# Kernel optimization log

Hardware: AMD Instinct MI355X
Metric: run time of the kernel (lower is better)

The kernel has to match this reference:

```python
import jax, jax.numpy as jnp
import numpy as np

DIM = 512
HEADS = 8
HD = DIM // HEADS          # head_dim = 64
GROUPS = 32                # GroupNorm groups
EPS = 1e-5
SCALE = HD ** -0.25        # double-scale: applied to both q and k
B, H, W, L, CTX = 8, 32, 32, 77, 768


def setup_inputs() -> dict:
    key = jax.random.key(0)
    ks = jax.random.split(key, 6)
    return {
        "x": jax.random.normal(ks[0], (B, DIM, H, W), jnp.float32),
        "context": jax.random.normal(ks[1], (B, L, CTX), jnp.float32),
        "gn_gamma": jnp.ones((DIM,), jnp.float32),
        "gn_beta": jnp.zeros((DIM,), jnp.float32),
        "qkv_w": jax.random.normal(ks[2], (3 * DIM, DIM), jnp.float32) * 0.02,
        "qkv_b": jnp.zeros((3 * DIM,), jnp.float32),
        "ckv_w": jax.random.normal(ks[3], (2 * DIM, CTX), jnp.float32) * 0.02,
        "ckv_b": jnp.zeros((2 * DIM,), jnp.float32),
        "proj_w": jax.random.normal(ks[4], (DIM, DIM), jnp.float32) * 0.02,
        "proj_b": jnp.zeros((DIM,), jnp.float32),
    }


def _group_norm(x, gamma, beta):
    b, c, h, w = x.shape
    xr = x.reshape(b, GROUPS, c // GROUPS, h, w)
    mu = xr.mean(axis=(2, 3, 4), keepdims=True)
    var = xr.var(axis=(2, 3, 4), keepdims=True)
    xr = (xr - mu) * jax.lax.rsqrt(var + EPS)
    return xr.reshape(b, c, h, w) * gamma[None, :, None, None] + beta[None, :, None, None]


def reference(x, context, gn_gamma, gn_beta, qkv_w, qkv_b, ckv_w, ckv_b, proj_w, proj_b):
    b, c, h, w = x.shape
    n, d = HEADS, HD
    identity = x

    xn = _group_norm(x, gn_gamma, gn_beta)
    # 1x1 conv == channel GEMM. qkv: [b, 3*dim, h*w] -> [b, 3, n, d, hw]
    qkv = jnp.einsum('bchw,oc->bohw', xn, qkv_w) + qkv_b[None, :, None, None]
    qkv = qkv.reshape(b, 3, n, d, h * w)
    q, k, v = qkv[:, 0], qkv[:, 1], qkv[:, 2]   # each [b, n, d, hw]

    # context kv: Linear(context_dim, 2*dim) -> [b, L, 2, n, d] -> [b, n, d, L]
    ckv = jnp.einsum('blc,oc->blo', context, ckv_w) + ckv_b
    ckv = ckv.reshape(b, -1, 2, n, d)
    ck = jnp.transpose(ckv[:, :, 0], (0, 2, 3, 1))  # [b, n, d, L]
    cv = jnp.transpose(ckv[:, :, 1], (0, 2, 3, 1))
    k = jnp.concatenate([ck, k], axis=-1)           # [b, n, d, L+hw]
    v = jnp.concatenate([cv, v], axis=-1)

    # attn = (q^T * s) @ (k * s); softmax over keys
    attn = jnp.einsum('bndq,bndk->bnqk', q * SCALE, k * SCALE)
    attn = jax.nn.softmax(attn, axis=-1)
    out = jnp.einsum('bndk,bnqk->bndq', v, attn).reshape(b, c, h, w)

    out = jnp.einsum('bchw,oc->bohw', out, proj_w) + proj_b[None, :, None, None]
    return out + identity
```

## Files before the change

### kernel.cpp

```cpp
#include <hip/hip_runtime.h>

#define B_ 8
#define DIM_ 512
#define HEADS_ 8
#define HD_ 64
#define HW_ 1024
#define L_ 77
#define LP_ 80
#define CTX_ 768
#define KV_ 1101
#define KVP_ 1152
#define NPAD_ 51
#define CTX0_ 1024
#define SC_QK 0.42466089f

typedef __attribute__((ext_vector_type(8))) short bf16x8;
typedef __attribute__((ext_vector_type(4))) float f32x4;
typedef __attribute__((ext_vector_type(4))) unsigned short u16x4;

__device__ __forceinline__ unsigned short f2bf(float f) {
  union { float f; unsigned int u; } c; c.f = f;
  unsigned int u = c.u;
  return (unsigned short)((u + 0x7fffu + ((u >> 16) & 1u)) >> 16);
}
__device__ __forceinline__ float bf2f(unsigned short h) {
  union { unsigned int u; float f; } c; c.u = ((unsigned int)h) << 16;
  return c.f;
}

#define GLD_LDS16(gsrc, ldst) \
  __builtin_amdgcn_global_load_lds((const __attribute__((address_space(1))) void*)(gsrc), \
                                   (__attribute__((address_space(3))) void*)(ldst), 16, 0, 0)

__global__ __launch_bounds__(256) void prep_k(const float* __restrict__ x,
                                              const float* __restrict__ gamma,
                                              const float* __restrict__ beta,
                                              const float* __restrict__ qkv_w,
                                              const float* __restrict__ ckv_w,
                                              const float* __restrict__ proj_w,
                                              const float* __restrict__ ctx,
                                              unsigned short* __restrict__ xn_t,
                                              unsigned short* __restrict__ dq,
                                              unsigned short* __restrict__ dc,
                                              unsigned short* __restrict__ dp,
                                              unsigned short* __restrict__ ctx_bf,
                                              unsigned short* __restrict__ k_s,
                                              unsigned short* __restrict__ vT) {
  __shared__ unsigned short xs[16][1032];
  __shared__ float red[8];
  int bid = blockIdx.x;
  int tid = threadIdx.x;
  if (bid < 256) {
    const int b = bid >> 5, g = bid & 31;
    const float* xp = x + ((size_t)b * DIM_ + g * 16) * HW_;
    float sum = 0.f, ssq = 0.f;
#pragma unroll
    for (int i = 0; i < 16; ++i) {
      float4 v = *(const float4*)&xp[i * HW_ + tid * 4];
      sum += v.x + v.y + v.z + v.w;
      ssq += v.x * v.x + v.y * v.y + v.z * v.z + v.w * v.w;
      xs[i][tid * 4 + 0] = f2bf(v.x);
      xs[i][tid * 4 + 1] = f2bf(v.y);
      xs[i][tid * 4 + 2] = f2bf(v.z);
      xs[i][tid * 4 + 3] = f2bf(v.w);
    }
#pragma unroll
    for (int off = 32; off >= 1; off >>= 1) {
      sum += __shfl_xor(sum, off, 64);
      ssq += __shfl_xor(ssq, off, 64);
    }
    if ((tid & 63) == 0) { red[(tid >> 6) * 2] = sum; red[(tid >> 6) * 2 + 1] = ssq; }
    __syncthreads();
    sum = red[0] + red[2] + red[4] + red[6];
    ssq = red[1] + red[3] + red[5] + red[7];
    float mu = sum * (1.f / 16384.f);
    float rstd = rsqrtf(ssq * (1.f / 16384.f) - mu * mu + 1e-5f);
    float a[16], c[16];
#pragma unroll
    for (int ci = 0; ci < 16; ++ci) {
      float gm = gamma[g * 16 + ci], bt = beta[g * 16 + ci];
      a[ci] = rstd * gm;
      c[ci] = bt - mu * rstd * gm;
    }
#pragma unroll
    for (int t = 0; t < 4; ++t) {
      int hw = tid + t * 256;
      unsigned short tmp[16];
#pragma unroll
      for (int ci = 0; ci < 16; ++ci)
        tmp[ci] = f2bf(bf2f(xs[ci][hw]) * a[ci] + c[ci]);
      unsigned int w[8];
#pragma unroll
      for (int j = 0; j < 8; ++j) w[j] = (unsigned int)tmp[2 * j] | ((unsigned int)tmp[2 * j + 1] << 16);
      unsigned short* dptr = &xn_t[((size_t)b * HW_ + hw) * DIM_ + g * 16];
      *(uint4*)dptr = make_uint4(w[0], w[1], w[2], w[3]);
      *(uint4*)(dptr + 8) = make_uint4(w[4], w[5], w[6], w[7]);
    }
  } else if (bid < 2048) {
    int i = (bid - 256) * 256 + tid;
    const float* src;
    unsigned short* dst;
    int off;
    if (i < 196608) { src = qkv_w; dst = dq; off = i; }
    else if (i < 393216) { src = ckv_w; dst = dc; off = i - 196608; }
    else { src = proj_w; dst = dp; off = i - 393216; }
    float4 v = *(const float4*)(src + (size_t)off * 4);
    u16x4 o;
    o[0] = f2bf(v.x); o[1] = f2bf(v.y); o[2] = f2bf(v.z); o[3] = f2bf(v.w);
    *(u16x4*)(dst + (size_t)off * 4) = o;
  } else if (bid < 2528) {
    int i = (bid - 2048) * 256 + tid;
    int idx = i * 4;
    int b = idx / (LP_ * CTX_);
    int rem = idx - b * (LP_ * CTX_);
    int l = rem / CTX_;
    int c = rem - l * CTX_;
    float4 v = make_float4(0.f, 0.f, 0.f, 0.f);
    if (l < L_) v = *(const float4*)&ctx[((size_t)b * L_ + l) * CTX_ + c];
    u16x4 o;
    o[0] = f2bf(v.x); o[1] = f2bf(v.y); o[2] = f2bf(v.z); o[3] = f2bf(v.w);
    *(u16x4*)(ctx_bf + idx) = o;
  } else {
    int i = (bid - 2528) * 256 + tid;
    int bh = i / (NPAD_ * 64);
    int rem = i - bh * (NPAD_ * 64);
    int row = KV_ + rem / 64;
    int d = rem & 63;
    k_s[((size_t)bh * KVP_ + row) * HD_ + d] = 0;
    vT[((size_t)bh * HD_ + d) * KVP_ + row] = 0;
  }
}

template <int MODE, int BM, int BN>
__device__ __forceinline__ void gemm_body(int bid,
                                          const unsigned short* __restrict__ A,
                                          const unsigned short* __restrict__ Bt,
                                          int M, int N, int K,
                                          const float* __restrict__ bias,
                                          unsigned short* __restrict__ out_q,
                                          unsigned short* __restrict__ out_k,
                                          unsigned short* __restrict__ out_v,
                                          const float* __restrict__ xres,
                                          float* __restrict__ outf,
                                          unsigned short* sm) {
  constexpr int MR = BM / 32;
  constexpr int NR = BN / 32;
  constexpr int AG = BM / 64;
  constexpr int BG = BN / 64;
  constexpr int SLOADS = AG + BG;
  unsigned short* As0 = sm;
  unsigned short* Bs0 = sm + 3 * BM * 32;
  const int tid = threadIdx.x;
  const int wid = tid >> 6, lane = tid & 63;
  const int lr = lane & 15, lg = lane >> 4;
  const int ntn = N / BN;
  const int tm = bid / ntn, tn = bid - tm * ntn;
  const int m0 = tm * BM, n0 = tn * BN;
  const int wr = wid >> 1, wc = wid & 1;
  f32x4 acc[MR][NR] = {};
  const int nkt = K >> 5;

  auto stage = [&](int bi, int kk) {
#pragma unroll
    for (int i = 0; i < AG; ++i) {
      int c = i * 256 + tid;
      int row = c >> 2, l = (c & 3) ^ ((row >> 1) & 3);
      GLD_LDS16(A + (size_t)(m0 + row) * K + kk + l * 8,
                As0 + (size_t)bi * BM * 32 + (size_t)c * 8);
    }
#pragma unroll
    for (int i = 0; i < BG; ++i) {
      int c = i * 256 + tid;
      int row = c >> 2, l = (c & 3) ^ ((row >> 1) & 3);
      GLD_LDS16(Bt + (size_t)(n0 + row) * K + kk + l * 8,
                Bs0 + (size_t)bi * BN * 32 + (size_t)c * 8);
    }
  };

  __builtin_amdgcn_sched_barrier(0);
  stage(0, 0);
  __builtin_amdgcn_sched_barrier(0);
  stage(1, 32);
  __builtin_amdgcn_sched_barrier(0);

  int cur = 0;
  for (int kt = 0; kt < nkt; ++kt) {
    if (kt < nkt - 1) {
      if constexpr (SLOADS == 4) asm volatile("s_waitcnt vmcnt(4)" ::: "memory");
      else                       asm volatile("s_waitcnt vmcnt(3)" ::: "memory");
    } else {
      asm volatile("s_waitcnt vmcnt(0)" ::: "memory");
    }
    __builtin_amdgcn_sched_barrier(0);
    __builtin_amdgcn_s_barrier();
    __builtin_amdgcn_sched_barrier(0);
    if (kt + 2 < nkt) stage(cur == 0 ? 2 : cur - 1, (kt + 2) << 5);
    const unsigned short* Ab = As0 + cur * BM * 32;
    const unsigned short* Bb = Bs0 + cur * BN * 32;
    bf16x8 af[MR], bf[NR];
#pragma unroll
    for (int mi = 0; mi < MR; ++mi) {
      int row = wr * (BM / 2) + mi * 16 + lr;
      af[mi] = *(const bf16x8*)&Ab[row * 32 + ((lg ^ ((row >> 1) & 3)) * 8)];
    }
#pragma unroll
    for (int nj = 0; nj < NR; ++nj) {
      int row = wc * (BN / 2) + nj * 16 + lr;
      bf[nj] = *(const bf16x8*)&Bb[row * 32 + ((lg ^ ((row >> 1) & 3)) * 8)];
    }
#pragma unroll
    for (int mi = 0; mi < MR; ++mi)
#pragma unroll
      for (int nj = 0; nj < NR; ++nj)
        acc[mi][nj] = __builtin_amdgcn_mfma_f32_16x16x32_bf16(af[mi], bf[nj], acc[mi][nj], 0, 0, 0);
    cur = (cur == 2) ? 0 : cur + 1;
  }

  if constexpr (MODE == 0) {
    __syncthreads();
    const int which = n0 >> 9;
    const int bb = m0 >> 10;
    const int qibase = m0 & 1023;
    if (which == 2) {
      uint2* Vt = (uint2*)sm;
#pragma unroll
      for (int mi = 0; mi < MR; ++mi) {
#pragma unroll
        for (int nj = 0; nj < NR; ++nj) {
          int col = wc * 64 + nj * 16 + lr;
          float b = bias[n0 + col];
          unsigned int w0, w1;
          float v0 = acc[mi][nj][0] + b, v1 = acc[mi][nj][1] + b;
          float v2 = acc[mi][nj][2] + b, v3 = acc[mi][nj][3] + b;
          asm("v_cvt_pk_bf16_f32 %0, %1, %2" : "=v"(w0) : "v"(v0), "v"(v1));
          asm("v_cvt_pk_bf16_f32 %0, %1, %2" : "=v"(w1) : "v"(v2), "v"(v3));
          int chunk = (wr * 16 + mi * 4 + lg) ^ (lr * 2);
          Vt[col * 32 + chunk] = make_uint2(w0, w1);
        }
      }
      __syncthreads();
#pragma unroll
      for (int it = 0; it < 8; ++it) {
        int col = wid * 32 + it * 4 + lg;
        uint4 val = *(uint4*)&Vt[col * 32 + ((lr * 2) ^ ((col & 15) * 2))];
        int colg = n0 + col;
        int head = (colg >> 6) & 7, d = colg & 63;
        *(uint4*)&out_v[(((size_t)bb * HEADS_ + head) * HD_ + d) * KVP_ + qibase + lr * 8] = val;
      }
    } else {
      unsigned short* Tq = sm;
#pragma unroll
      for (int mi = 0; mi < MR; ++mi) {
#pragma unroll
        for (int nj = 0; nj < NR; ++nj) {
          int col = wc * 64 + nj * 16 + lr;
          float b = bias[n0 + col];
          int qr = wr * 64 + mi * 16 + lg * 4;
#pragma unroll
          for (int r = 0; r < 4; ++r)
            Tq[(qr + r) * 132 + col] = f2bf((acc[mi][nj][r] + b) * SC_QK);
        }
      }
      __syncthreads();
#pragma unroll
      for (int it = 0; it < 8; ++it) {
        int qi = wid * 32 + it * 4 + lg;
        uint2 lo = *(uint2*)&Tq[qi * 132 + lr * 8];
        uint2 hi = *(uint2*)&Tq[qi * 132 + lr * 8 + 4];
        uint4 val = make_uint4(lo.x, lo.y, hi.x, hi.y);
        int colg = n0 + lr * 8;
        int head = (colg >> 6) & 7, d = colg & 63;
        size_t bh = (size_t)bb * HEADS_ + head;
        if (which == 0)
          *(uint4*)&out_q[(bh * HW_ + qibase + qi) * HD_ + d] = val;
        else
          *(uint4*)&out_k[(bh * KVP_ + qibase + qi) * HD_ + d] = val;
      }
    }
  } else {
#pragma unroll
    for (int mi = 0; mi < MR; ++mi) {
#pragma unroll
      for (int nj = 0; nj < NR; ++nj) {
#pragma unroll
        for (int r = 0; r < 4; ++r) {
          int row = m0 + wr * (BM / 2) + mi * 16 + lg * 4 + r;
          int col = n0 + wc * (BN / 2) + nj * 16 + lr;
          float v = acc[mi][nj][r];
          if (MODE == 1) {
            int bb = row / LP_, l = row - bb * LP_;
            if (l < L_) {
              v += bias[col];
              int which = col >> 9, head = (col >> 6) & 7, d = col & 63;
              size_t bh = (size_t)bb * HEADS_ + head;
              if (which == 0) out_k[(bh * KVP_ + CTX0_ + l) * HD_ + d] = f2bf(v * SC_QK);
              else            out_v[(bh * HD_ + d) * KVP_ + CTX0_ + l] = f2bf(v);
            }
          } else {
            size_t idx = (size_t)(col >> 10) * (DIM_ * HW_) + (size_t)row * HW_ + (col & 1023);
            outf[idx] = v + bias[row] + xres[idx];
          }
        }
      }
    }
  }
}

__global__ __launch_bounds__(256, 3) void gemm_qkv_ckv_k(
    const unsigned short* __restrict__ xn_t, const unsigned short* __restrict__ qkvw,
    const unsigned short* __restrict__ ctx_bf, const unsigned short* __restrict__ ckvw,
    const float* __restrict__ qkv_b, const float* __restrict__ ckv_b,
    unsigned short* __restrict__ q_s, unsigned short* __restrict__ k_s,
    unsigned short* __restrict__ vT) {
  __shared__ unsigned short sm[3 * 256 * 32];
  int bid = blockIdx.x;
  if (bid < 80) {
    gemm_body<1, 64, 128>(bid, ctx_bf, ckvw, 640, 1024, 768, ckv_b,
                          nullptr, k_s, vT, nullptr, nullptr, sm);
  } else {
    int b = bid - 80;
    int b2 = (b & 7) * 96 + (b >> 3);
    gemm_body<0, 128, 128>(b2, xn_t, qkvw, 8192, 1536, 512, qkv_b,
                           q_s, k_s, vT, nullptr, nullptr, sm);
  }
}

__global__ __launch_bounds__(256, 4) void gemm_proj_k(
    const unsigned short* __restrict__ projw, const unsigned short* __restrict__ at_s,
    const float* __restrict__ proj_b, const float* __restrict__ x,
    float* __restrict__ out) {
  __shared__ unsigned short sm[3 * 192 * 32];
  gemm_body<2, 64, 128>(blockIdx.x, projw, at_s, 512, 8192, 512, proj_b,
                        nullptr, nullptr, nullptr, x, out, sm);
}

#define PSTRIDE 72

__device__ __forceinline__ void attn_tile64(const unsigned short* __restrict__ Ksb,
                                            const unsigned short* __restrict__ Vsb,
                                            const bf16x8 (&qf)[2], const bf16x8 ones,
                                            unsigned short* __restrict__ Pw,
                                            int lr, int lg,
                                            const int (&ro)[4], const int (&koff)[2],
                                            f32x4& lacc, f32x4 (&acc)[4]) {
  f32x4 st[4] = {};
  __builtin_amdgcn_s_setprio(1);
#pragma unroll
  for (int ks = 0; ks < 2; ++ks) {
    bf16x8 kf[4];
#pragma unroll
    for (int t = 0; t < 4; ++t)
      kf[t] = *(const bf16x8*)&Ksb[ro[t] + koff[ks]];
#pragma unroll
    for (int t = 0; t < 4; ++t)
      st[t] = __builtin_amdgcn_mfma_f32_16x16x32_bf16(kf[t], qf[ks], st[t], 0, 0, 0);
  }
  __builtin_amdgcn_s_setprio(0);
#pragma unroll
  for (int t = 0; t < 4; ++t)
#pragma unroll
    for (int r = 0; r < 4; ++r) st[t][r] = __builtin_amdgcn_exp2f(st[t][r]);
#pragma unroll
  for (int t = 0; t < 4; ++t) {
    unsigned int w0, w1;
    asm("v_cvt_pk_bf16_f32 %0, %1, %2" : "=v"(w0) : "v"(st[t][0]), "v"(st[t][1]));
    asm("v_cvt_pk_bf16_f32 %0, %1, %2" : "=v"(w1) : "v"(st[t][2]), "v"(st[t][3]));
    *(uint2*)&Pw[lr * PSTRIDE + t * 16 + lg * 4] = make_uint2(w0, w1);
  }
#pragma unroll
  for (int ks = 0; ks < 2; ++ks) {
    bf16x8 pb = *(const bf16x8*)&Pw[lr * PSTRIDE + ks * 32 + lg * 8];
    __builtin_amdgcn_s_setprio(1);
    lacc = __builtin_amdgcn_mfma_f32_16x16x32_bf16(ones, pb, lacc, 0, 0, 0);
#pragma unroll
    for (int dt = 0; dt < 4; ++dt) {
      bf16x8 vf = *(const bf16x8*)&Vsb[ro[dt] + koff[ks]];
      acc[dt] = __builtin_amdgcn_mfma_f32_16x16x32_bf16(vf, pb, acc[dt], 0, 0, 0);
    }
    __builtin_amdgcn_s_setprio(0);
  }
}

__global__ __launch_bounds__(512, 4) void attn_k(const unsigned short* __restrict__ q_s,
                                                 const unsigned short* __restrict__ k_s,
                                                 const unsigned short* __restrict__ vT,
                                                 unsigned short* __restrict__ at_s) {
  __shared__ unsigned short Ks[3][4096];
  __shared__ unsigned short Vs[3][4096];
  __shared__ unsigned short Pb[8][16 * PSTRIDE];
  const int tid = threadIdx.x;
  const int wid = tid >> 6, lane = tid & 63;
  const int lr = lane & 15, lg = lane >> 4;
  const int bidx = blockIdx.x;
  const int xcd = bidx & 7, idx = bidx >> 3;
  const int bh = xcd + 8 * (idx >> 3);
  const int qt = idx & 7;
  const int q0 = qt * 128 + wid * 16;
  const unsigned short* qp = q_s + (size_t)bh * HW_ * HD_;
  const unsigned short* kp = k_s + (size_t)bh * KVP_ * HD_;
  const unsigned short* vp = vT + (size_t)bh * HD_ * KVP_;
  unsigned short* Pw = Pb[wid];

  const int srow = lane >> 3;
  const int schunk = (lane & 7) ^ srow;

  auto stage = [&](int bufi, int kk) {
    if (wid < 4) {
#pragma unroll
      for (int jj = 0; jj < 2; ++jj)
        GLD_LDS16(kp + (size_t)(kk + wid * 16 + jj * 8 + srow) * HD_ + schunk * 8,
                  &Ks[bufi][(wid * 2 + jj) * 512]);
    } else {
#pragma unroll
      for (int jj = 0; jj < 2; ++jj)
        GLD_LDS16(vp + (size_t)((wid - 4) * 16 + jj * 8 + srow) * KVP_ + kk + schunk * 8,
                  &Vs[bufi][((wid - 4) * 2 + jj) * 512]);
    }
  };

  int ro[4], koff[2];
#pragma unroll
  for (int t = 0; t < 4; ++t) ro[t] = (t * 16 + lr) * 64;
#pragma unroll
  for (int ks = 0; ks < 2; ++ks) koff[ks] = ((ks * 4 + lg) ^ (lr & 7)) * 8;

  bf16x8 qf[2];
#pragma unroll
  for (int ks = 0; ks < 2; ++ks)
    qf[ks] = *(const bf16x8*)&qp[(size_t)(q0 + lr) * HD_ + ks * 32 + lg * 8];

  bf16x8 ones;
#pragma unroll
  for (int j = 0; j < 8; ++j) ones[j] = (short)0x3F80;

  f32x4 acc[4] = {};
  f32x4 lacc = {};

  __builtin_amdgcn_sched_barrier(0);
  stage(0, 0);
  __builtin_amdgcn_sched_barrier(0);
  stage(1, 64);
  __builtin_amdgcn_sched_barrier(0);

  for (int it = 0; it < 18; ++it) {
    if (it < 17) {
      asm volatile("s_waitcnt vmcnt(2)" ::: "memory");
    } else {
      asm volatile("s_waitcnt vmcnt(0)" ::: "memory");
    }
    __builtin_amdgcn_sched_barrier(0);
    __builtin_amdgcn_s_barrier();
    __builtin_amdgcn_sched_barrier(0);
    if (it + 2 < 18) {
      int bi = it + 2;
      stage(bi - (bi / 3) * 3, bi * 64);
    }
    int cb = it - (it / 3) * 3;
    attn_tile64(Ks[cb], Vs[cb], qf, ones, Pw, lr, lg, ro, koff, lacc, acc);
  }

  const int bb = bh >> 3, head = bh & 7;
  const float inv = 1.f / (lacc[0] - (float)NPAD_);
  const int qi = q0 + lr;
#pragma unroll
  for (int dt = 0; dt < 4; ++dt) {
    u16x4 o;
#pragma unroll
    for (int r = 0; r < 4; ++r) o[r] = f2bf(acc[dt][r] * inv);
    *(u16x4*)&at_s[((size_t)bb * HW_ + qi) * DIM_ + head * HD_ + dt * 16 + lg * 4] = o;
  }
}

extern "C" void kernel_launch(void* const* d_in, const int* in_sizes, int n_in,
                              void* d_out, int out_size, void* d_ws, size_t ws_size,
                              hipStream_t stream) {
  (void)in_sizes; (void)n_in; (void)out_size; (void)ws_size;
  const float* x      = (const float*)d_in[0];
  const float* ctx    = (const float*)d_in[1];
  const float* gng    = (const float*)d_in[2];
  const float* gnb    = (const float*)d_in[3];
  const float* qkv_w  = (const float*)d_in[4];
  const float* qkv_b  = (const float*)d_in[5];
  const float* ckv_w  = (const float*)d_in[6];
  const float* ckv_b  = (const float*)d_in[7];
  const float* proj_w = (const float*)d_in[8];
  const float* proj_b = (const float*)d_in[9];
  float* out = (float*)d_out;

  char* ws = (char*)d_ws;
  size_t off = 0;
  auto alloc = [&](size_t bytes) {
    char* p = ws + off;
    off = (off + bytes + 255) & ~(size_t)255;
    return p;
  };
  unsigned short* xn_t    = (unsigned short*)alloc((size_t)B_ * HW_ * DIM_ * 2);
  unsigned short* ctx_bf  = (unsigned short*)alloc((size_t)B_ * LP_ * CTX_ * 2);
  unsigned short* qkvw_bf = (unsigned short*)alloc((size_t)3 * DIM_ * DIM_ * 2);
  unsigned short* ckvw_bf = (unsigned short*)alloc((size_t)2 * DIM_ * CTX_ * 2);
  unsigned short* projw_bf= (unsigned short*)alloc((size_t)DIM_ * DIM_ * 2);
  unsigned short* q_s     = (unsigned short*)alloc((size_t)64 * HW_ * HD_ * 2);
  unsigned short* k_s     = (unsigned short*)alloc((size_t)64 * KVP_ * HD_ * 2);
  unsigned short* vT      = (unsigned short*)alloc((size_t)64 * HD_ * KVP_ * 2);
  unsigned short* at_s    = (unsigned short*)alloc((size_t)B_ * HW_ * DIM_ * 2);

  prep_k<<<3344, 256, 0, stream>>>(x, gng, gnb, qkv_w, ckv_w, proj_w, ctx,
                                   xn_t, qkvw_bf, ckvw_bf, projw_bf, ctx_bf, k_s, vT);
  gemm_qkv_ckv_k<<<848, 256, 0, stream>>>(xn_t, qkvw_bf, ctx_bf, ckvw_bf,
                                          qkv_b, ckv_b, q_s, k_s, vT);
  attn_k<<<512, 512, 0, stream>>>(q_s, k_s, vT, at_s);
  gemm_proj_k<<<512, 256, 0, stream>>>(projw_bf, at_s, proj_b, x, out);
}
```

Baseline: 77.00 us.

## Software-pipeline attention: overlap next tile's QK MFMA with current softmax and PV

Splits the attention tile into a QK score stage and a softmax+PV stage, then unrolls the key loop by two so the QK MFMAs for tile i+1 are issued before the exp/convert/PV work of tile i. V staging gets a fourth LDS buffer because V tiles now stay live one iteration longer. The aim is to hide exp and LDS round-trip latency behind matrix work, at the cost of more registers (two score sets) and extra LDS, which may reduce occupancy.

```diff
diff --git a/kernel.cpp b/kernel.cpp
--- a/kernel.cpp
+++ b/kernel.cpp
@@ -336,14 +336,12 @@
 
 #define PSTRIDE 72
 
-__device__ __forceinline__ void attn_tile64(const unsigned short* __restrict__ Ksb,
-                                            const unsigned short* __restrict__ Vsb,
-                                            const bf16x8 (&qf)[2], const bf16x8 ones,
-                                            unsigned short* __restrict__ Pw,
-                                            int lr, int lg,
-                                            const int (&ro)[4], const int (&koff)[2],
-                                            f32x4& lacc, f32x4 (&acc)[4]) {
-  f32x4 st[4] = {};
+__device__ __forceinline__ void attn_qk(const unsigned short* __restrict__ Ksb,
+                                        const bf16x8 (&qf)[2],
+                                        const int (&ro)[4], const int (&koff)[2],
+                                        f32x4 (&st)[4]) {
+#pragma unroll
+  for (int t = 0; t < 4; ++t) st[t] = (f32x4){0.f, 0.f, 0.f, 0.f};
   __builtin_amdgcn_s_setprio(1);
 #pragma unroll
   for (int ks = 0; ks < 2; ++ks) {
@@ -356,6 +354,15 @@
       st[t] = __builtin_amdgcn_mfma_f32_16x16x32_bf16(kf[t], qf[ks], st[t], 0, 0, 0);
   }
   __builtin_amdgcn_s_setprio(0);
+}
+
+__device__ __forceinline__ void attn_smpv(f32x4 (&st)[4],
+                                          const unsigned short* __restrict__ Vsb,
+                                          const bf16x8 ones,
+                                          unsigned short* __restrict__ Pw,
+                                          int lr, int lg,
+                                          const int (&ro)[4], const int (&koff)[2],
+                                          f32x4& lacc, f32x4 (&acc)[4]) {
 #pragma unroll
   for (int t = 0; t < 4; ++t)
 #pragma unroll
@@ -386,7 +393,7 @@
                                                  const unsigned short* __restrict__ vT,
                                                  unsigned short* __restrict__ at_s) {
   __shared__ unsigned short Ks[3][4096];
-  __shared__ unsigned short Vs[3][4096];
+  __shared__ unsigned short Vs[4][4096];
   __shared__ unsigned short Pb[8][16 * PSTRIDE];
   const int tid = threadIdx.x;
   const int wid = tid >> 6, lane = tid & 63;
@@ -404,17 +411,17 @@
   const int srow = lane >> 3;
   const int schunk = (lane & 7) ^ srow;
 
-  auto stage = [&](int bufi, int kk) {
+  auto stage = [&](int kslot, int vslot, int kk) {
     if (wid < 4) {
 #pragma unroll
       for (int jj = 0; jj < 2; ++jj)
         GLD_LDS16(kp + (size_t)(kk + wid * 16 + jj * 8 + srow) * HD_ + schunk * 8,
-                  &Ks[bufi][(wid * 2 + jj) * 512]);
+                  &Ks[kslot][(wid * 2 + jj) * 512]);
     } else {
 #pragma unroll
       for (int jj = 0; jj < 2; ++jj)
         GLD_LDS16(vp + (size_t)((wid - 4) * 16 + jj * 8 + srow) * KVP_ + kk + schunk * 8,
-                  &Vs[bufi][((wid - 4) * 2 + jj) * 512]);
+                  &Vs[vslot][((wid - 4) * 2 + jj) * 512]);
     }
   };
 
@@ -435,29 +442,34 @@
 
   f32x4 acc[4] = {};
   f32x4 lacc = {};
+  f32x4 stA[4], stB[4];
 
   __builtin_amdgcn_sched_barrier(0);
-  stage(0, 0);
+  stage(0, 0, 0);
   __builtin_amdgcn_sched_barrier(0);
-  stage(1, 64);
+  stage(1, 1, 64);
   __builtin_amdgcn_sched_barrier(0);
 
-  for (int it = 0; it < 18; ++it) {
-    if (it < 17) {
-      asm volatile("s_waitcnt vmcnt(2)" ::: "memory");
-    } else {
-      asm volatile("s_waitcnt vmcnt(0)" ::: "memory");
-    }
+  for (int j = 0; j < 9; ++j) {
+    const int it0 = 2 * j, it1 = it0 + 1;
+    if (it0 < 17) asm volatile("s_waitcnt vmcnt(2)" ::: "memory");
+    else          asm volatile("s_waitcnt vmcnt(0)" ::: "memory");
     __builtin_amdgcn_sched_barrier(0);
     __builtin_amdgcn_s_barrier();
     __builtin_amdgcn_sched_barrier(0);
-    if (it + 2 < 18) {
-      int bi = it + 2;
-      stage(bi - (bi / 3) * 3, bi * 64);
-    }
-    int cb = it - (it / 3) * 3;
-    attn_tile64(Ks[cb], Vs[cb], qf, ones, Pw, lr, lg, ro, koff, lacc, acc);
-  }
+    if (it0 + 2 < 18) stage((it0 + 2) % 3, (it0 + 2) & 3, (it0 + 2) * 64);
+    attn_qk(Ks[it0 % 3], qf, ro, koff, stA);
+    if (j > 0)
+      attn_smpv(stB, Vs[(it0 - 1) & 3], ones, Pw, lr, lg, ro, koff, lacc, acc);
+    asm volatile("s_waitcnt vmcnt(2)" ::: "memory");
+    __builtin_amdgcn_sched_barrier(0);
+    __builtin_amdgcn_s_barrier();
+    __builtin_amdgcn_sched_barrier(0);
+    if (it1 + 2 < 18) stage((it1 + 2) % 3, (it1 + 2) & 3, (it1 + 2) * 64);
+    attn_qk(Ks[it1 % 3], qf, ro, koff, stB);
+    attn_smpv(stA, Vs[it0 & 3], ones, Pw, lr, lg, ro, koff, lacc, acc);
+  }
+  attn_smpv(stB, Vs[17 & 3], ones, Pw, lr, lg, ro, koff, lacc, acc);
 
   const int bb = bh >> 3, head = bh & 7;
   const float inv = 1.f / (lacc[0] - (float)NPAD_);
```

After: 76.42 us. Within noise of the previous version (-0.8%).
